# Performance work log

Measured on AMD Instinct MI355X. Metric: run time of the kernel, lower is better.

## Reference

```python
import math
import jax, jax.numpy as jnp
import numpy as np

NUM_FREQ = 10  # NeRF-style L=10 -> enc dim 3 + 3*2*10 = 63

def pos_encode(coords):
    # freq_bands = 2^i * pi, i = 0..L-1
    freq = (2.0 ** jnp.arange(NUM_FREQ, dtype=coords.dtype)) * math.pi
    scaled = coords[..., None] * freq                      # [E, 3, L]
    enc = jnp.stack([jnp.sin(scaled), jnp.cos(scaled)], axis=-1)  # [E, 3, L, 2]
    enc = enc.reshape(coords.shape[0], -1)                 # [E, 60] interleaved sin/cos
    return jnp.concatenate([coords, enc], axis=-1)         # [E, 63]

def setup_inputs() -> dict:
    key = jax.random.key(0)
    ks = jax.random.split(key, 9)
    N, M, K, C = 65536, 16384, 32, 64
    E = M * K
    x = jax.random.normal(ks[0], (N, C), jnp.float32)
    pos = jax.random.normal(ks[1], (N, 3), jnp.float32)
    batch = jnp.sort(jax.random.randint(ks[2], (N,), 0, 8))
    idx = jax.random.randint(ks[3], (M,), 0, N)
    row = jnp.sort(jax.random.randint(ks[4], (E,), 0, M))
    col = jax.random.randint(ks[5], (E,), 0, N)
    d_in = C + 3 + 3 * 2 * NUM_FREQ  # 127
    def lin(k, i, o):
        s = 1.0 / np.sqrt(i)
        kw, kb = jax.random.split(k)
        return (jax.random.uniform(kw, (i, o), jnp.float32, -s, s),
                jax.random.uniform(kb, (o,), jnp.float32, -s, s))
    lw1, lb1 = lin(ks[6], d_in, 128)
    lw2, lb2 = lin(ks[7], 128, 128)
    gw, gb = lin(ks[8], 128, 256)
    return dict(x=x, pos=pos, batch=batch, idx=idx, row=row, col=col,
                lw1=lw1, lb1=lb1, lw2=lw2, lb2=lb2, gw=gw, gb=gb)

def reference(x, pos, batch, idx, row, col, lw1, lb1, lw2, lb2, gw, gb):
    M = idx.shape[0]
    pos_idx = pos[idx]                         # [M, 3] sampled centers
    pos_diff = pos[col] - pos_idx[row]         # [E, 3] neighbor offsets
    pe = pos_encode(pos_diff)                  # [E, 63]
    edge_in = jnp.concatenate([x[col], pe], axis=-1)   # [E, 127]
    # local_nn: Linear->ReLU->Linear (no final activation, per MLP_Wrapper)
    h = jax.nn.relu(edge_in @ lw1 + lb1)       # [E, 128]
    edge_feat = h @ lw2 + lb2                  # [E, 128]
    # scatter_reduce amax, include_self=False: empty rows stay 0
    agg = jax.ops.segment_max(edge_feat, row, num_segments=M)
    agg = jnp.where(jnp.isneginf(agg), jnp.zeros((), agg.dtype), agg)
    out = agg @ gw + gb                        # [M, 256] global_nn (single Linear)
    return out, pos_idx, batch[idx]
```

## Files before the change

kernel.cpp:

```cpp
#include <hip/hip_runtime.h>
#include <math.h>

#define NN 65536
#define MM 16384
#define EE 524288
#define CF 64
#define HD 128
#define OD 256
#define RPB 16
#define PITCH 129

typedef __bf16 bf16x8 __attribute__((ext_vector_type(8)));
typedef __bf16 bf16x4 __attribute__((ext_vector_type(4)));
typedef float f32x4 __attribute__((ext_vector_type(4)));

__device__ __forceinline__ unsigned enc_f(float f) {
    unsigned u = __float_as_uint(f);
    return (u & 0x80000000u) ? ~u : (u | 0x80000000u);
}
__device__ __forceinline__ float dec_f(unsigned e) {
    unsigned u = (e & 0x80000000u) ? (e ^ 0x80000000u) : ~e;
    return __uint_as_float(u);
}
#define ENC_NEG_INF 0x007FFFFFu

__device__ __forceinline__ unsigned bf_bits(float f) {
    __bf16 b = (__bf16)f;
    return (unsigned)__builtin_bit_cast(unsigned short, b);
}

__global__ void k_wprep(__bf16* __restrict__ fragbuf,
                        const float* __restrict__ lw1, const float* __restrict__ lw2) {
    const int t = threadIdx.x;
    const int lane = t & 63;
    const int wv = t >> 6;
    const int q = lane >> 4;
    const int ln = lane & 15;
    #pragma unroll
    for (int fi = 0; fi < 16; ++fi) {
        const int nt = (fi >> 2) & 1, kk = fi & 3;
        const int n = wv * 32 + nt * 16 + ln;
        bf16x8 f;
        #pragma unroll
        for (int j = 0; j < 8; ++j) {
            const int c = kk * 32 + q * 8 + j;
            const int rk = (c < 67) ? c : c - 1;
            f[j] = (fi < 8) ? (__bf16)((c == 67) ? 0.0f : lw1[rk * HD + n])
                            : (__bf16)lw2[c * HD + n];
        }
        *(bf16x8*)&fragbuf[((size_t)fi * 256 + t) * 8] = f;
    }
}

__global__ void k_prep(const float* __restrict__ pos, const int* __restrict__ batch,
                       const int* __restrict__ idx, float* __restrict__ out) {
    int m = blockIdx.x * 256 + threadIdx.x;
    if (m >= MM) return;
    int s = idx[m];
    out[MM * OD + m * 3 + 0] = pos[s * 3 + 0];
    out[MM * OD + m * 3 + 1] = pos[s * 3 + 1];
    out[MM * OD + m * 3 + 2] = pos[s * 3 + 2];
    out[MM * OD + MM * 3 + m] = (float)batch[s];
}

__launch_bounds__(256)
__global__ void k_fused(const float* __restrict__ x, const float* __restrict__ pos,
                        const int* __restrict__ idx, const int* __restrict__ row,
                        const int* __restrict__ col, const __bf16* __restrict__ fragbuf,
                        const float* __restrict__ lb1, const float* __restrict__ lb2,
                        const float* __restrict__ gw, const float* __restrict__ gb,
                        float* __restrict__ out) {
    __shared__ __align__(16) __bf16 ein[2][64][HD];
    __shared__ __align__(16) __bf16 hbuf[64][HD];
    __shared__ unsigned maxbuf[(RPB + 1) * PITCH];
    __shared__ int srow[2][64];
    const int t = threadIdx.x;
    const int lane = t & 63;
    const int wv = t >> 6;
    const int q = lane >> 4;
    const int ln = lane & 15;
    const int lsw = ln & 7;
    const int m0 = blockIdx.x * RPB;

    auto lbound = [&](int target) {
        int lo = 0, hi = EE;
        while (lo < hi) { int mid = (lo + hi) >> 1; if (row[mid] < target) lo = mid + 1; else hi = mid; }
        return lo;
    };
    const int es = lbound(m0);
    const int ee = lbound(m0 + RPB);
    const int ntiles = (ee - es + 63) >> 6;

    for (int i = t; i < (RPB + 1) * PITCH; i += 256) maxbuf[i] = ENC_NEG_INF;

    const int pe_e = t >> 2, pe_part = t & 3, pe_esw = pe_e & 7;
    float4 v0, v1, v2, v3;
    auto issue = [&](int tt) {
        const int eg = min(es + tt * 64 + pe_e, EE - 1);
        const int c = col[eg];
        const float4* xr = (const float4*)(x + (size_t)c * CF) + pe_part * 4;
        v0 = xr[0]; v1 = xr[1]; v2 = xr[2]; v3 = xr[3];
    };
    auto commit = [&](int b) {
        bf16x8 pk;
        pk[0] = (__bf16)v0.x; pk[1] = (__bf16)v0.y; pk[2] = (__bf16)v0.z; pk[3] = (__bf16)v0.w;
        pk[4] = (__bf16)v1.x; pk[5] = (__bf16)v1.y; pk[6] = (__bf16)v1.z; pk[7] = (__bf16)v1.w;
        *(bf16x8*)&ein[b][pe_e][((pe_part * 2 + 0) ^ pe_esw) * 8] = pk;
        pk[0] = (__bf16)v2.x; pk[1] = (__bf16)v2.y; pk[2] = (__bf16)v2.z; pk[3] = (__bf16)v2.w;
        pk[4] = (__bf16)v3.x; pk[5] = (__bf16)v3.y; pk[6] = (__bf16)v3.z; pk[7] = (__bf16)v3.w;
        *(bf16x8*)&ein[b][pe_e][((pe_part * 2 + 1) ^ pe_esw) * 8] = pk;
    };
    auto do_pe = [&](int tt) {
        if (t < 192) {
            const int e = t & 63, d = t >> 6;
            const int b = tt & 1;
            const int eidx = es + tt * 64 + e;
            const int eg = min(eidx, EE - 1);
            const int r = row[eg];
            const int c = col[eg];
            const int s = idx[r];
            const int esw = e & 7;
            const float pd = pos[c * 3 + d] - pos[s * 3 + d];
            if (d == 0) {
                srow[b][e] = (eidx < ee) ? (r - m0) : RPB;
                const float pd1 = pos[c * 3 + 1] - pos[s * 3 + 1];
                const float pd2 = pos[c * 3 + 2] - pos[s * 3 + 2];
                uint2 pkt;
                pkt.x = bf_bits(pd) | (bf_bits(pd1) << 16);
                pkt.y = bf_bits(pd2);
                *(uint2*)&ein[b][e][(8 ^ esw) * 8] = pkt;
            }
            const float fr = __builtin_amdgcn_fractf(pd * 0.5f);
            float sv = __builtin_amdgcn_sinf(fr);
            float cv = __builtin_amdgcn_cosf(fr);
            #pragma unroll
            for (int l = 0; l < 10; ++l) {
                const int colp = 68 + d * 20 + l * 2;
                *(unsigned*)&ein[b][e][((colp >> 3) ^ esw) * 8 + (colp & 7)] =
                    bf_bits(sv) | (bf_bits(cv) << 16);
                const float s2 = 2.0f * sv * cv;
                const float c2 = 1.0f - 2.0f * sv * sv;
                sv = s2; cv = c2;
            }
        }
    };

    if (ntiles > 0) issue(0);

    bf16x8 w1f[2][4];
    #pragma unroll
    for (int nt = 0; nt < 2; ++nt)
        #pragma unroll
        for (int kk = 0; kk < 4; ++kk)
            w1f[nt][kk] = *(const bf16x8*)&fragbuf[((size_t)(nt * 4 + kk) * 256 + t) * 8];
    float4 b1q[2];
    #pragma unroll
    for (int nt = 0; nt < 2; ++nt)
        b1q[nt] = *(const float4*)&lb1[wv * 32 + nt * 16 + q * 4];

    if (ntiles > 0) {
        commit(0);
        do_pe(0);
        if (ntiles > 1) issue(1);
    }
    __syncthreads();

    for (int tt = 0; tt < ntiles; ++tt) {
        const int p = tt & 1;

        f32x4 acc[2][4];
        #pragma unroll
        for (int nt = 0; nt < 2; ++nt)
            #pragma unroll
            for (int et = 0; et < 4; ++et)
                acc[nt][et] = (f32x4){b1q[nt].x, b1q[nt].y, b1q[nt].z, b1q[nt].w};
        #pragma unroll
        for (int et = 0; et < 4; ++et) {
            const int e = et * 16 + ln;
            #pragma unroll
            for (int kk = 0; kk < 4; ++kk) {
                bf16x8 a = *(const bf16x8*)&ein[p][e][((kk * 4 + q) ^ lsw) * 8];
                acc[0][et] = __builtin_amdgcn_mfma_f32_16x16x32_bf16(w1f[0][kk], a, acc[0][et], 0, 0, 0);
                acc[1][et] = __builtin_amdgcn_mfma_f32_16x16x32_bf16(w1f[1][kk], a, acc[1][et], 0, 0, 0);
            }
        }
        if (tt + 1 < ntiles) { commit(p ^ 1); do_pe(tt + 1); }
        if (tt + 2 < ntiles) issue(tt + 2);
        #pragma unroll
        for (int et = 0; et < 4; ++et) {
            const int e = et * 16 + ln;
            #pragma unroll
            for (int nt = 0; nt < 2; ++nt) {
                bf16x4 hv;
                hv[0] = (__bf16)fmaxf(acc[nt][et][0], 0.0f);
                hv[1] = (__bf16)fmaxf(acc[nt][et][1], 0.0f);
                hv[2] = (__bf16)fmaxf(acc[nt][et][2], 0.0f);
                hv[3] = (__bf16)fmaxf(acc[nt][et][3], 0.0f);
                const int chunk = wv * 4 + nt * 2 + (q >> 1);
                *(bf16x4*)&hbuf[e][((chunk ^ lsw) * 8) + (q & 1) * 4] = hv;
            }
        }
        __syncthreads();

        {
            bf16x8 w2f[2][4];
            #pragma unroll
            for (int nt = 0; nt < 2; ++nt)
                #pragma unroll
                for (int kk = 0; kk < 4; ++kk)
                    w2f[nt][kk] = *(const bf16x8*)&fragbuf[((size_t)(8 + nt * 4 + kk) * 256 + t) * 8];

            f32x4 acc2[4][2];
            #pragma unroll
            for (int nt = 0; nt < 2; ++nt) {
                const float b2 = lb2[wv * 32 + nt * 16 + ln];
                #pragma unroll
                for (int et = 0; et < 4; ++et)
                    acc2[et][nt] = (f32x4){b2, b2, b2, b2};
            }
            #pragma unroll
            for (int et = 0; et < 4; ++et) {
                const int e = et * 16 + ln;
                #pragma unroll
                for (int kk = 0; kk < 4; ++kk) {
                    bf16x8 ah = *(const bf16x8*)&hbuf[e][((kk * 4 + q) ^ lsw) * 8];
                    acc2[et][0] = __builtin_amdgcn_mfma_f32_16x16x32_bf16(ah, w2f[0][kk], acc2[et][0], 0, 0, 0);
                    acc2[et][1] = __builtin_amdgcn_mfma_f32_16x16x32_bf16(ah, w2f[1][kk], acc2[et][1], 0, 0, 0);
                }
            }
            const int sb = tt & 1;
            #pragma unroll
            for (int et = 0; et < 4; ++et) {
                const int4 R = *(const int4*)&srow[sb][et * 16 + q * 4];
                #pragma unroll
                for (int nt = 0; nt < 2; ++nt) {
                    unsigned* base = maxbuf + (wv * 32 + nt * 16 + ln);
                    const f32x4 vv = acc2[et][nt];
                    int cur = R.x;
                    float m = vv[0];
                    if (R.y != cur) { atomicMax(base + cur * PITCH, enc_f(m)); cur = R.y; m = vv[1]; }
                    else m = fmaxf(m, vv[1]);
                    if (R.z != cur) { atomicMax(base + cur * PITCH, enc_f(m)); cur = R.z; m = vv[2]; }
                    else m = fmaxf(m, vv[2]);
                    if (R.w != cur) { atomicMax(base + cur * PITCH, enc_f(m)); cur = R.w; m = vv[3]; }
                    else m = fmaxf(m, vv[3]);
                    atomicMax(base + cur * PITCH, enc_f(m));
                }
            }
        }
        __syncthreads();
    }

    float* afin = (float*)hbuf;
    for (int i = t; i < RPB * HD; i += 256) {
        const unsigned e = maxbuf[(i >> 7) * PITCH + (i & 127)];
        afin[i] = (e == ENC_NEG_INF) ? 0.0f : dec_f(e);
    }
    __syncthreads();

    const int j4 = (t & 63) * 4;
    const int rbase = (t >> 6) * 4;
    float facc[4][4];
    const float4 bias = *(const float4*)&gb[j4];
    #pragma unroll
    for (int r = 0; r < 4; ++r) { facc[r][0] = bias.x; facc[r][1] = bias.y; facc[r][2] = bias.z; facc[r][3] = bias.w; }
    for (int k = 0; k < 128; k += 4) {
        float4 w0 = *(const float4*)&gw[(k + 0) * OD + j4];
        float4 w1 = *(const float4*)&gw[(k + 1) * OD + j4];
        float4 w2 = *(const float4*)&gw[(k + 2) * OD + j4];
        float4 w3 = *(const float4*)&gw[(k + 3) * OD + j4];
        #pragma unroll
        for (int r = 0; r < 4; ++r) {
            float4 av = *(const float4*)&afin[(rbase + r) * HD + k];
            facc[r][0] += av.x * w0.x + av.y * w1.x + av.z * w2.x + av.w * w3.x;
            facc[r][1] += av.x * w0.y + av.y * w1.y + av.z * w2.y + av.w * w3.y;
            facc[r][2] += av.x * w0.z + av.y * w1.z + av.z * w2.z + av.w * w3.z;
            facc[r][3] += av.x * w0.w + av.y * w1.w + av.z * w2.w + av.w * w3.w;
        }
    }
    #pragma unroll
    for (int r = 0; r < 4; ++r) {
        float4 v; v.x = facc[r][0]; v.y = facc[r][1]; v.z = facc[r][2]; v.w = facc[r][3];
        *(float4*)&out[(size_t)(m0 + rbase + r) * OD + j4] = v;
    }
}

extern "C" void kernel_launch(void* const* d_in, const int* in_sizes, int n_in,
                              void* d_out, int out_size, void* d_ws, size_t ws_size,
                              hipStream_t stream) {
    const float* x   = (const float*)d_in[0];
    const float* pos = (const float*)d_in[1];
    const int* batch = (const int*)d_in[2];
    const int* idx   = (const int*)d_in[3];
    const int* row   = (const int*)d_in[4];
    const int* col   = (const int*)d_in[5];
    const float* lw1 = (const float*)d_in[6];
    const float* lb1 = (const float*)d_in[7];
    const float* lw2 = (const float*)d_in[8];
    const float* lb2 = (const float*)d_in[9];
    const float* gw  = (const float*)d_in[10];
    const float* gb  = (const float*)d_in[11];
    float* out = (float*)d_out;
    __bf16* fragbuf = (__bf16*)d_ws;

    hipLaunchKernelGGL(k_wprep, dim3(1), dim3(256), 0, stream, fragbuf, lw1, lw2);
    hipLaunchKernelGGL(k_prep, dim3((MM + 255) / 256), dim3(256), 0, stream, pos, batch, idx, out);
    hipLaunchKernelGGL(k_fused, dim3(MM / RPB), dim3(256), 0, stream,
                       x, pos, idx, row, col, fragbuf, lb1, lb2, gw, gb, out);
}
```

Measured before the change: 117.1 us.

## Precompute row pointers, merge prep kernels, split edge LDS buffer and reschedule PE

The two setup kernels become one launch, which also computes a CSR row-pointer array, so each fused block reads its edge range instead of doing two binary searches. The edge-input LDS tile is split into a double-buffered x part and a single-buffered positional-encoding part, which reduces shared memory. Positional-encoding computation for the next tile moves after the second GEMM, where it can overlap MFMA work. This depends on the single PE buffer being safely synchronised between tiles, and it adds workspace use for the row pointers.

```diff
diff --git a/kernel.cpp b/kernel.cpp
--- a/kernel.cpp
+++ b/kernel.cpp
@@ -29,48 +29,64 @@
     return (unsigned)__builtin_bit_cast(unsigned short, b);
 }
 
-__global__ void k_wprep(__bf16* __restrict__ fragbuf,
-                        const float* __restrict__ lw1, const float* __restrict__ lw2) {
+#define WS_FRAG_OFF 0
+#define WS_ROWPTR_OFF 65536
+
+__global__ void k_pre(__bf16* __restrict__ fragbuf, int* __restrict__ rowptr,
+                      const float* __restrict__ lw1, const float* __restrict__ lw2,
+                      const int* __restrict__ row,
+                      const float* __restrict__ pos, const int* __restrict__ batch,
+                      const int* __restrict__ idx, float* __restrict__ out) {
+    const int b = blockIdx.x;
     const int t = threadIdx.x;
-    const int lane = t & 63;
-    const int wv = t >> 6;
-    const int q = lane >> 4;
-    const int ln = lane & 15;
-    #pragma unroll
-    for (int fi = 0; fi < 16; ++fi) {
-        const int nt = (fi >> 2) & 1, kk = fi & 3;
-        const int n = wv * 32 + nt * 16 + ln;
-        bf16x8 f;
-        #pragma unroll
-        for (int j = 0; j < 8; ++j) {
-            const int c = kk * 32 + q * 8 + j;
-            const int rk = (c < 67) ? c : c - 1;
-            f[j] = (fi < 8) ? (__bf16)((c == 67) ? 0.0f : lw1[rk * HD + n])
-                            : (__bf16)lw2[c * HD + n];
-        }
-        *(bf16x8*)&fragbuf[((size_t)fi * 256 + t) * 8] = f;
-    }
-}
-
-__global__ void k_prep(const float* __restrict__ pos, const int* __restrict__ batch,
-                       const int* __restrict__ idx, float* __restrict__ out) {
-    int m = blockIdx.x * 256 + threadIdx.x;
-    if (m >= MM) return;
-    int s = idx[m];
-    out[MM * OD + m * 3 + 0] = pos[s * 3 + 0];
-    out[MM * OD + m * 3 + 1] = pos[s * 3 + 1];
-    out[MM * OD + m * 3 + 2] = pos[s * 3 + 2];
-    out[MM * OD + MM * 3 + m] = (float)batch[s];
+    if (b == 0) {
+        const int lane = t & 63;
+        const int wv = t >> 6;
+        const int q = lane >> 4;
+        const int ln = lane & 15;
+        #pragma unroll
+        for (int fi = 0; fi < 16; ++fi) {
+            const int nt = (fi >> 2) & 1, kk = fi & 3;
+            const int n = wv * 32 + nt * 16 + ln;
+            bf16x8 f;
+            #pragma unroll
+            for (int j = 0; j < 8; ++j) {
+                const int c = kk * 32 + q * 8 + j;
+                const int rk = (c < 67) ? c : c - 1;
+                f[j] = (fi < 8) ? (__bf16)((c == 67) ? 0.0f : lw1[rk * HD + n])
+                                : (__bf16)lw2[c * HD + n];
+            }
+            *(bf16x8*)&fragbuf[((size_t)fi * 256 + t) * 8] = f;
+        }
+    } else if (b <= 65) {
+        const int i = (b - 1) * 256 + t;
+        if (i <= MM) {
+            int lo = 0, hi = EE;
+            while (lo < hi) { int mid = (lo + hi) >> 1; if (row[mid] < i) lo = mid + 1; else hi = mid; }
+            rowptr[i] = lo;
+        }
+    } else {
+        const int m = (b - 66) * 256 + t;
+        if (m < MM) {
+            const int s = idx[m];
+            out[MM * OD + m * 3 + 0] = pos[s * 3 + 0];
+            out[MM * OD + m * 3 + 1] = pos[s * 3 + 1];
+            out[MM * OD + m * 3 + 2] = pos[s * 3 + 2];
+            out[MM * OD + MM * 3 + m] = (float)batch[s];
+        }
+    }
 }
 
 __launch_bounds__(256)
 __global__ void k_fused(const float* __restrict__ x, const float* __restrict__ pos,
                         const int* __restrict__ idx, const int* __restrict__ row,
-                        const int* __restrict__ col, const __bf16* __restrict__ fragbuf,
+                        const int* __restrict__ col, const int* __restrict__ rowptr,
+                        const __bf16* __restrict__ fragbuf,
                         const float* __restrict__ lb1, const float* __restrict__ lb2,
                         const float* __restrict__ gw, const float* __restrict__ gb,
                         float* __restrict__ out) {
-    __shared__ __align__(16) __bf16 ein[2][64][HD];
+    __shared__ __align__(16) __bf16 einX[2][64][64];
+    __shared__ __align__(16) __bf16 einP[64][64];
     __shared__ __align__(16) __bf16 hbuf[64][HD];
     __shared__ unsigned maxbuf[(RPB + 1) * PITCH];
     __shared__ int srow[2][64];
@@ -82,13 +98,8 @@
     const int lsw = ln & 7;
     const int m0 = blockIdx.x * RPB;
 
-    auto lbound = [&](int target) {
-        int lo = 0, hi = EE;
-        while (lo < hi) { int mid = (lo + hi) >> 1; if (row[mid] < target) lo = mid + 1; else hi = mid; }
-        return lo;
-    };
-    const int es = lbound(m0);
-    const int ee = lbound(m0 + RPB);
+    const int es = rowptr[m0];
+    const int ee = rowptr[m0 + RPB];
     const int ntiles = (ee - es + 63) >> 6;
 
     for (int i = t; i < (RPB + 1) * PITCH; i += 256) maxbuf[i] = ENC_NEG_INF;
@@ -105,15 +116,15 @@
         bf16x8 pk;
         pk[0] = (__bf16)v0.x; pk[1] = (__bf16)v0.y; pk[2] = (__bf16)v0.z; pk[3] = (__bf16)v0.w;
         pk[4] = (__bf16)v1.x; pk[5] = (__bf16)v1.y; pk[6] = (__bf16)v1.z; pk[7] = (__bf16)v1.w;
-        *(bf16x8*)&ein[b][pe_e][((pe_part * 2 + 0) ^ pe_esw) * 8] = pk;
+        *(bf16x8*)&einX[b][pe_e][((pe_part * 2 + 0) ^ pe_esw) * 8] = pk;
         pk[0] = (__bf16)v2.x; pk[1] = (__bf16)v2.y; pk[2] = (__bf16)v2.z; pk[3] = (__bf16)v2.w;
         pk[4] = (__bf16)v3.x; pk[5] = (__bf16)v3.y; pk[6] = (__bf16)v3.z; pk[7] = (__bf16)v3.w;
-        *(bf16x8*)&ein[b][pe_e][((pe_part * 2 + 1) ^ pe_esw) * 8] = pk;
+        *(bf16x8*)&einX[b][pe_e][((pe_part * 2 + 1) ^ pe_esw) * 8] = pk;
     };
     auto do_pe = [&](int tt) {
         if (t < 192) {
             const int e = t & 63, d = t >> 6;
-            const int b = tt & 1;
+            const int sb = tt & 1;
             const int eidx = es + tt * 64 + e;
             const int eg = min(eidx, EE - 1);
             const int r = row[eg];
@@ -122,21 +133,21 @@
             const int esw = e & 7;
             const float pd = pos[c * 3 + d] - pos[s * 3 + d];
             if (d == 0) {
-                srow[b][e] = (eidx < ee) ? (r - m0) : RPB;
+                srow[sb][e] = (eidx < ee) ? (r - m0) : RPB;
                 const float pd1 = pos[c * 3 + 1] - pos[s * 3 + 1];
                 const float pd2 = pos[c * 3 + 2] - pos[s * 3 + 2];
                 uint2 pkt;
                 pkt.x = bf_bits(pd) | (bf_bits(pd1) << 16);
                 pkt.y = bf_bits(pd2);
-                *(uint2*)&ein[b][e][(8 ^ esw) * 8] = pkt;
+                *(uint2*)&einP[e][esw * 8] = pkt;
             }
             const float fr = __builtin_amdgcn_fractf(pd * 0.5f);
             float sv = __builtin_amdgcn_sinf(fr);
             float cv = __builtin_amdgcn_cosf(fr);
             #pragma unroll
             for (int l = 0; l < 10; ++l) {
-                const int colp = 68 + d * 20 + l * 2;
-                *(unsigned*)&ein[b][e][((colp >> 3) ^ esw) * 8 + (colp & 7)] =
+                const int jP = 4 + d * 20 + l * 2;
+                *(unsigned*)&einP[e][((jP >> 3) ^ esw) * 8 + (jP & 7)] =
                     bf_bits(sv) | (bf_bits(cv) << 16);
                 const float s2 = 2.0f * sv * cv;
                 const float c2 = 1.0f - 2.0f * sv * sv;
@@ -177,14 +188,18 @@
         #pragma unroll
         for (int et = 0; et < 4; ++et) {
             const int e = et * 16 + ln;
+            bf16x8 a[4];
+            a[0] = *(const bf16x8*)&einX[p][e][(q ^ lsw) * 8];
+            a[1] = *(const bf16x8*)&einX[p][e][((4 + q) ^ lsw) * 8];
+            a[2] = *(const bf16x8*)&einP[e][(q ^ lsw) * 8];
+            a[3] = *(const bf16x8*)&einP[e][((4 + q) ^ lsw) * 8];
             #pragma unroll
             for (int kk = 0; kk < 4; ++kk) {
-                bf16x8 a = *(const bf16x8*)&ein[p][e][((kk * 4 + q) ^ lsw) * 8];
-                acc[0][et] = __builtin_amdgcn_mfma_f32_16x16x32_bf16(w1f[0][kk], a, acc[0][et], 0, 0, 0);
-                acc[1][et] = __builtin_amdgcn_mfma_f32_16x16x32_bf16(w1f[1][kk], a, acc[1][et], 0, 0, 0);
-            }
-        }
-        if (tt + 1 < ntiles) { commit(p ^ 1); do_pe(tt + 1); }
+                acc[0][et] = __builtin_amdgcn_mfma_f32_16x16x32_bf16(w1f[0][kk], a[kk], acc[0][et], 0, 0, 0);
+                acc[1][et] = __builtin_amdgcn_mfma_f32_16x16x32_bf16(w1f[1][kk], a[kk], acc[1][et], 0, 0, 0);
+            }
+        }
+        if (tt + 1 < ntiles) commit(p ^ 1);
         if (tt + 2 < ntiles) issue(tt + 2);
         #pragma unroll
         for (int et = 0; et < 4; ++et) {
@@ -228,6 +243,7 @@
                     acc2[et][1] = __builtin_amdgcn_mfma_f32_16x16x32_bf16(ah, w2f[1][kk], acc2[et][1], 0, 0, 0);
                 }
             }
+            if (tt + 1 < ntiles) do_pe(tt + 1);
             const int sb = tt & 1;
             #pragma unroll
             for (int et = 0; et < 4; ++et) {
@@ -301,10 +317,11 @@
     const float* gw  = (const float*)d_in[10];
     const float* gb  = (const float*)d_in[11];
     float* out = (float*)d_out;
-    __bf16* fragbuf = (__bf16*)d_ws;
-
-    hipLaunchKernelGGL(k_wprep, dim3(1), dim3(256), 0, stream, fragbuf, lw1, lw2);
-    hipLaunchKernelGGL(k_prep, dim3((MM + 255) / 256), dim3(256), 0, stream, pos, batch, idx, out);
+    __bf16* fragbuf = (__bf16*)((char*)d_ws + WS_FRAG_OFF);
+    int* rowptr     = (int*)((char*)d_ws + WS_ROWPTR_OFF);
+
+    hipLaunchKernelGGL(k_pre, dim3(1 + 65 + 64), dim3(256), 0, stream,
+                       fragbuf, rowptr, lw1, lw2, row, pos, batch, idx, out);
     hipLaunchKernelGGL(k_fused, dim3(MM / RPB), dim3(256), 0, stream,
-                       x, pos, idx, row, col, fragbuf, lb1, lb2, gw, gb, out);
-}
+                       x, pos, idx, row, col, rowptr, fragbuf, lb1, lb2, gw, gb, out);
+}
```

Result: faster. 102.5 us (-12.5%).
